# Performance work log

Measured on AMD Instinct MI355X. Metric: run time of the kernel, lower is better.

The kernel has to match this reference:

```python
import jax, jax.numpy as jnp
import numpy as np

B, C, H, W = 4, 64, 256, 256
WIDE = 256      # num_features * width_multiplier
K = 4           # dynamic kernel banks
KS = 3          # kernel size
RED = 16        # channels // reduction = 64 // 4
PAD = KS // 2


def _wn(v, g):
    # torch weight_norm, dim=0: norm over all dims except leading dim
    n = jnp.sqrt(jnp.sum(v * v, axis=tuple(range(1, v.ndim)), keepdims=True))
    return g * v / n


def _conv(x, w, groups=1):
    return jax.lax.conv_general_dilated(
        x, w, window_strides=(1, 1), padding=[(PAD, PAD), (PAD, PAD)],
        feature_group_count=groups, dimension_numbers=('NCHW', 'OIHW', 'NCHW'))


def setup_inputs() -> dict:
    key = jax.random.key(0)
    ks = jax.random.split(key, 16)
    s = lambda k, shape, sc: jax.random.normal(k, shape, jnp.float32) * sc
    return {
        'x': jax.random.normal(ks[0], (B, C, H, W), jnp.float32),
        'scale': jax.random.uniform(ks[1], (B, 1), jnp.float32, 1.0, 4.0),
        # body conv 1 (weight-normed, ReLU)
        'v1': s(ks[2], (WIDE, C, KS, KS), 0.05), 'g1': jnp.ones((WIDE, 1, 1, 1), jnp.float32),
        'b1': jnp.zeros((WIDE,), jnp.float32),
        # body conv 2 (weight-normed, no act)
        'v2': s(ks[3], (C, WIDE, KS, KS), 0.05), 'g2': jnp.ones((C, 1, 1, 1), jnp.float32),
        'b2': jnp.zeros((C,), jnp.float32),
        # scale-aware dynamic conv: K banks of [C_out, C_in, k, k], weight-normed over dim 0 (=K)
        'dyn_v': s(ks[4], (K, C, C, KS, KS), 0.05), 'dyn_g': jnp.ones((K, 1, 1, 1, 1), jnp.float32),
        'dyn_b': jnp.zeros((K, C), jnp.float32),
        # routing: Linear(1 -> K) + softmax
        'att_w': s(ks[5], (1, K), 1.0), 'att_b': jnp.zeros((K,), jnp.float32),
        # SE block: Linear(C -> C/red, no bias), ReLU, Linear(C/red -> C, no bias), Sigmoid
        'se_w1': s(ks[6], (RED, C), 0.1), 'se_w2': s(ks[7], (C, RED), 0.1),
    }


def reference(x, scale, v1, g1, b1, v2, g2, b2, dyn_v, dyn_g, dyn_b,
              att_w, att_b, se_w1, se_w2):
    # --- body: wide weight-normed conv stack ---
    r = jax.nn.relu(_conv(x, _wn(v1, g1)) + b1[None, :, None, None])   # [B,WIDE,H,W]
    r = _conv(r, _wn(v2, g2)) + b2[None, :, None, None]                # [B,C,H,W]
    # --- scale-aware dynamic conv: per-sample softmax mix of K kernels ---
    att = jax.nn.softmax(scale @ att_w + att_b, axis=-1)               # [B,K]
    w_bank = _wn(dyn_v, dyn_g)                                         # [K,C,C,k,k]
    w_b = jnp.einsum('bk,koicd->boicd', att, w_bank)                   # [B,C,C,k,k]
    bias_b = att @ dyn_b                                               # [B,C]
    # batch-grouped conv: one distinct kernel per sample
    y = _conv(r.reshape(1, B * C, H, W), w_b.reshape(B * C, C, KS, KS), groups=B)
    y = y.reshape(B, C, H, W) + bias_b[:, :, None, None]
    # --- SE gating ---
    p = jnp.mean(y, axis=(2, 3))                                       # [B,C]
    gate = jax.nn.sigmoid(jax.nn.relu(p @ se_w1.T) @ se_w2.T)          # [B,C]
    y = y * gate[:, :, None, None]
    # --- residual ---
    return x + y
```

## Files before the change

kernel.cpp:

```cpp
#include <hip/hip_runtime.h>

typedef __attribute__((ext_vector_type(8))) short short8;
typedef __attribute__((ext_vector_type(4))) float f32x4;

#define HH 256
#define WW 256

__device__ inline unsigned int f2bf(float x) {
  unsigned int u = __float_as_uint(x);
  return (u + 0x7fffu + ((u >> 16) & 1u)) >> 16;
}
__device__ inline unsigned int pack2(float a, float b) {
  return f2bf(a) | (f2bf(b) << 16);
}

__global__ __launch_bounds__(256) void xpose_k(const float* __restrict__ x,
                                               unsigned short* __restrict__ xcl) {
  const int t = threadIdx.x;
  const int ci = t & 63;
  const int wv = t >> 6;
  const int x0 = blockIdx.x * 64;
  const int y  = blockIdx.y;
  const int b  = blockIdx.z;
  const float* src = x + ((size_t)(b * 64 + ci) * HH + y) * WW + x0 + wv;
  unsigned short* dst = xcl + ((size_t)(b * HH + y) * WW + x0 + wv) * 64 + ci;
#pragma unroll
  for (int k = 0; k < 16; ++k)
    dst[(size_t)k * 4 * 64] = (unsigned short)f2bf(src[4 * k]);
}

template <int COUT, int CINK>
__global__ __launch_bounds__(256) void wnorm_k(const float* __restrict__ v,
                                               const float* __restrict__ g,
                                               unsigned short* __restrict__ out) {
  constexpr int N = CINK * 9;
  const int co = blockIdx.x, t = threadIdx.x;
  const float* vb = v + (size_t)co * N;
  float s = 0.f;
  for (int i = t; i < N; i += 256) { float a = vb[i]; s += a * a; }
  for (int off = 32; off > 0; off >>= 1) s += __shfl_xor(s, off, 64);
  __shared__ float red[4];
  if ((t & 63) == 0) red[t >> 6] = s;
  __syncthreads();
  const float tot = red[0] + red[1] + red[2] + red[3];
  const float sc = g[co] / sqrtf(tot);
  for (int i = t; i < N; i += 256) {
    int ci = i / 9, tap = i - 9 * (i / 9);
    out[((size_t)tap * COUT + co) * CINK + ci] = (unsigned short)f2bf(vb[i] * sc);
  }
}

__global__ __launch_bounds__(256) void dynnorm_k(const float* __restrict__ dyn_v,
                                                 const float* __restrict__ dyn_g,
                                                 float* __restrict__ dscale) {
  const int k = blockIdx.x, t = threadIdx.x;
  const float* vb = dyn_v + (size_t)k * 36864;
  float s = 0.f;
  for (int i = t; i < 36864; i += 256) { float a = vb[i]; s += a * a; }
  for (int off = 32; off > 0; off >>= 1) s += __shfl_xor(s, off, 64);
  __shared__ float red[4];
  if ((t & 63) == 0) red[t >> 6] = s;
  __syncthreads();
  if (t == 0) dscale[k] = dyn_g[k] / sqrtf(red[0] + red[1] + red[2] + red[3]);
}

__global__ __launch_bounds__(256) void mix_k(const float* __restrict__ scale,
                                             const float* __restrict__ att_w,
                                             const float* __restrict__ att_b,
                                             const float* __restrict__ dyn_v,
                                             const float* __restrict__ dyn_b,
                                             const float* __restrict__ dscale,
                                             unsigned short* __restrict__ wbt,
                                             float* __restrict__ bias_b,
                                             float* __restrict__ zp) {
  const int blk = blockIdx.x;
  const int b = blk >> 6, co = blk & 63;
  const int t = threadIdx.x;
  float att[4], wsc[4];
  const float sc = scale[b];
  float mx = -1e30f;
#pragma unroll
  for (int k = 0; k < 4; ++k) { att[k] = sc * att_w[k] + att_b[k]; mx = fmaxf(mx, att[k]); }
  float den = 0.f;
#pragma unroll
  for (int k = 0; k < 4; ++k) { att[k] = expf(att[k] - mx); den += att[k]; }
#pragma unroll
  for (int k = 0; k < 4; ++k) { att[k] /= den; wsc[k] = att[k] * dscale[k]; }
  for (int i = t; i < 576; i += 256) {
    int ci = i / 9, tap = i - 9 * (i / 9);
    float w = 0.f;
#pragma unroll
    for (int k = 0; k < 4; ++k)
      w += wsc[k] * dyn_v[(((size_t)k * 64 + co) * 64 + ci) * 9 + tap];
    wbt[(((size_t)b * 9 + tap) * 64 + co) * 64 + ci] = (unsigned short)f2bf(w);
  }
  if (t == 0) {
    float bb = 0.f;
#pragma unroll
    for (int k = 0; k < 4; ++k) bb += att[k] * dyn_b[k * 64 + co];
    bias_b[blk] = bb;
  }
  if (blk == 0) zp[t] = 0.f;
}

template <int CIN, int COUT, int OSTR, bool RELU, bool DYN>
__global__ __launch_bounds__(256, 2) void conv3x3_mfma(const unsigned short* __restrict__ in_cl,
                                                       const unsigned short* __restrict__ wt,
                                                       const float* __restrict__ bias,
                                                       unsigned short* __restrict__ out_cl,
                                                       float* __restrict__ y_out,
                                                       float* __restrict__ pblk,
                                                       const float* __restrict__ zp) {
  constexpr int CO_TILES = COUT / 64;
  constexpr int NCH = CIN / 32;
  constexpr int NSLOT = 612 * 4;
  const int tid = threadIdx.x;
  const int lane = tid & 63;
  const int wv = tid >> 6;
  const int l15 = lane & 15;
  const int lg = lane >> 4;

  const int wg = (blockIdx.x & 7) * (gridDim.x >> 3) + (blockIdx.x >> 3);
  int tdec = wg;
  const int cot = tdec % CO_TILES; tdec /= CO_TILES;
  const int bx = tdec & 7; tdec >>= 3;
  const int by = tdec & 15; tdec >>= 4;
  const int bz = tdec;

  const int x0 = bx * 32;
  const int y0 = by * 16;
  const int co0 = cot * 64;

  const unsigned short* inb = in_cl + (size_t)bz * HH * WW * CIN;
  const unsigned short* wtb = wt + (DYN ? (size_t)bz * 9 * 64 * 64 : (size_t)0);
  const float* biasb = bias + (DYN ? bz * 64 : 0);
  const unsigned short* zp16 = (const unsigned short*)zp;

  __shared__ unsigned short tile[NSLOT * 8];
  __shared__ unsigned short atile[2304 * 8];

  const unsigned short* sptr[10];
  bool sact[10];
#pragma unroll
  for (int k = 0; k < 10; ++k) {
    const int u = k * 256 + tid;
    const int pair = u >> 3;
    const int s = ((u & 7) * 16) ^ ((pair & 7) << 4);
    const int parity = s >> 6;
    const int g = (s >> 4) & 3;
    const int px = 2 * pair + parity;
    const int row = px / 34, col = px - 34 * row;
    const int gy = y0 - 1 + row, gx = x0 - 1 + col;
    sact[k] = (u < NSLOT);
    const bool ok = sact[k] && ((unsigned)gy < (unsigned)HH) && ((unsigned)gx < (unsigned)WW);
    sptr[k] = ok ? (inb + ((size_t)(gy * WW + gx)) * CIN + g * 8) : zp16;
  }

  f32x4 acc[4][8];
#pragma unroll
  for (int m = 0; m < 4; ++m)
#pragma unroll
    for (int n = 0; n < 8; ++n) acc[m][n] = (f32x4){0.f, 0.f, 0.f, 0.f};

#pragma unroll 1
  for (int ch = 0; ch < NCH; ++ch) {
    if (ch) __syncthreads();
#pragma unroll
    for (int k = 0; k < 10; ++k) {
      if (sact[k])
        __builtin_amdgcn_global_load_lds((const void*)(sptr[k] + ch * 32),
                                         (void*)(tile + (size_t)(k * 256 + wv * 64) * 8),
                                         16, 0, 0);
    }
#pragma unroll
    for (int k = 0; k < 9; ++k) {
      const int idx = k * 256 + tid;
      const int tap = idx >> 8;
      const int g = (idx >> 6) & 3;
      const int co = idx & 63;
      __builtin_amdgcn_global_load_lds(
          (const void*)(wtb + ((size_t)(tap * COUT + co0 + co) * CIN + ch * 32 + g * 8)),
          (void*)(atile + (size_t)(k * 256 + wv * 64) * 8), 16, 0, 0);
    }
    __syncthreads();

#pragma unroll
    for (int dx = 0; dx < 3; ++dx) {
      short8 Af[3][4];
#pragma unroll
      for (int dy = 0; dy < 3; ++dy)
#pragma unroll
        for (int m = 0; m < 4; ++m)
          Af[dy][m] = *(const short8*)((const char*)atile +
                                       (((dy * 3 + dx) * 4 + lg) * 1024 + (16 * m + l15) * 16));
#pragma unroll
      for (int ch2 = 0; ch2 < 2; ++ch2) {
#pragma unroll
        for (int bi = 0; bi < 6; ++bi) {
          const int px = (4 * wv + bi) * 34 + 16 * ch2 + l15 + dx;
          const int byt = (px >> 1) * 128 + ((lg * 16 + (px & 1) * 64) ^ (((px >> 1) & 7) << 4));
          const short8 Bv = *(const short8*)((const char*)tile + byt);
          const int dy_lo = (bi > 3) ? (bi - 3) : 0;
          const int dy_hi = (bi < 2) ? bi : 2;
          __builtin_amdgcn_s_setprio(1);
#pragma unroll
          for (int dy = 0; dy < 3; ++dy) {
            if (dy < dy_lo || dy > dy_hi) continue;
            const int n = 2 * (bi - dy) + ch2;
#pragma unroll
            for (int m = 0; m < 4; ++m)
              acc[m][n] = __builtin_amdgcn_mfma_f32_16x16x32_bf16(Af[dy][m], Bv, acc[m][n], 0, 0, 0);
          }
          __builtin_amdgcn_s_setprio(0);
        }
      }
    }
  }

  float scol[4][4];
  if (DYN) {
#pragma unroll
    for (int m = 0; m < 4; ++m)
#pragma unroll
      for (int f = 0; f < 4; ++f) scol[m][f] = 0.f;
  }

#pragma unroll
  for (int m = 0; m < 4; ++m) {
    const f32x4 bs = *(const f32x4*)(biasb + co0 + 16 * m + 4 * lg);
#pragma unroll
    for (int n = 0; n < 8; ++n) {
      f32x4 v = acc[m][n] + bs;
      if (RELU) {
        v.x = fmaxf(v.x, 0.f); v.y = fmaxf(v.y, 0.f);
        v.z = fmaxf(v.z, 0.f); v.w = fmaxf(v.w, 0.f);
      }
      const int yy = y0 + 4 * wv + (n >> 1);
      const int xx = x0 + 16 * (n & 1) + l15;
      if (!DYN) {
        uint2 pk;
        pk.x = pack2(v.x, v.y);
        pk.y = pack2(v.z, v.w);
        *(uint2*)(out_cl + (size_t)bz * HH * WW * OSTR +
                  ((size_t)(yy * WW + xx)) * OSTR + co0 + 16 * m + 4 * lg) = pk;
      } else {
        const size_t base = ((size_t)(bz * 64 + 16 * m + 4 * lg) * HH + yy) * WW + xx;
        y_out[base]             = v.x;
        y_out[base + 1 * 65536] = v.y;
        y_out[base + 2 * 65536] = v.z;
        y_out[base + 3 * 65536] = v.w;
        scol[m][0] += v.x; scol[m][1] += v.y; scol[m][2] += v.z; scol[m][3] += v.w;
      }
    }
  }
  if (DYN) {
#pragma unroll
    for (int m = 0; m < 4; ++m)
#pragma unroll
      for (int f = 0; f < 4; ++f) {
        float r = scol[m][f];
        r += __shfl_xor(r, 1, 64);
        r += __shfl_xor(r, 2, 64);
        r += __shfl_xor(r, 4, 64);
        r += __shfl_xor(r, 8, 64);
        scol[m][f] = r;
      }
    __syncthreads();
    float* red = (float*)tile;
    if (l15 == 0) {
#pragma unroll
      for (int m = 0; m < 4; ++m)
#pragma unroll
        for (int f = 0; f < 4; ++f)
          red[wv * 64 + 16 * m + 4 * lg + f] = scol[m][f];
    }
    __syncthreads();
    if (tid < 64) {
      const float s = red[tid] + red[64 + tid] + red[128 + tid] + red[192 + tid];
      pblk[((size_t)bz * 128 + by * 8 + bx) * 64 + tid] = s;
    }
  }
}

__global__ __launch_bounds__(256) void gate_k(const float* __restrict__ pblk,
                                              const float* __restrict__ se_w1,
                                              const float* __restrict__ se_w2,
                                              float* __restrict__ gate) {
  const int b = blockIdx.x;
  const int t = threadIdx.x;
  const int c = t & 63, part = t >> 6;
  __shared__ float ps[4][64];
  __shared__ float p_s[64], h_s[16];
  float s = 0.f;
  for (int blk = part; blk < 128; blk += 4)
    s += pblk[((size_t)b * 128 + blk) * 64 + c];
  ps[part][c] = s;
  __syncthreads();
  if (t < 64) p_s[t] = (ps[0][t] + ps[1][t] + ps[2][t] + ps[3][t]) * (1.f / 65536.f);
  __syncthreads();
  if (t < 16) {
    float h = 0.f;
    for (int cc = 0; cc < 64; ++cc) h += p_s[cc] * se_w1[t * 64 + cc];
    h_s[t] = fmaxf(h, 0.f);
  }
  __syncthreads();
  if (t < 64) {
    float a = 0.f;
    for (int j = 0; j < 16; ++j) a += h_s[j] * se_w2[t * 16 + j];
    gate[b * 64 + t] = 1.f / (1.f + expf(-a));
  }
}

__global__ __launch_bounds__(256) void final_k(const float* __restrict__ x,
                                               const float* __restrict__ gate,
                                               float* __restrict__ out) {
  const size_t i = ((size_t)blockIdx.x * 256 + threadIdx.x) * 4;
  f32x4 yv = *(f32x4*)(out + i);
  const f32x4 xv = *(const f32x4*)(x + i);
  const float g = gate[(int)(i >> 16)];
  yv = xv + yv * g;
  *(f32x4*)(out + i) = yv;
}

static constexpr size_t SZ_XCL = (size_t)4 * 256 * 256 * 64 * 2;
static constexpr size_t SZ_W   = (size_t)9 * 256 * 64 * 2;
static constexpr size_t SZ_PBLK = (size_t)4 * 128 * 64 * 4;

static constexpr size_t B_XCL = 0;
static constexpr size_t B_R   = B_XCL + SZ_XCL;
static constexpr size_t B_W1T = B_R + 4 * SZ_XCL;
static constexpr size_t B_W2T = B_W1T + SZ_W;
static constexpr size_t B_WBT = B_W2T + SZ_W;
static constexpr size_t B_DSC = B_WBT + SZ_W;
static constexpr size_t B_BB  = B_DSC + 256;
static constexpr size_t B_GT  = B_BB + 1024;
static constexpr size_t B_ZP  = B_GT + 1024;
static constexpr size_t B_PBLK = B_ZP + 1024;
static constexpr size_t WS_BIG = B_PBLK + SZ_PBLK;

extern "C" void kernel_launch(void* const* d_in, const int* in_sizes, int n_in,
                              void* d_out, int out_size, void* d_ws, size_t ws_size,
                              hipStream_t stream) {
  (void)in_sizes; (void)n_in; (void)out_size;
  if (ws_size < WS_BIG) return;

  const float* x     = (const float*)d_in[0];
  const float* scale = (const float*)d_in[1];
  const float* v1    = (const float*)d_in[2];
  const float* g1    = (const float*)d_in[3];
  const float* b1    = (const float*)d_in[4];
  const float* v2    = (const float*)d_in[5];
  const float* g2    = (const float*)d_in[6];
  const float* b2    = (const float*)d_in[7];
  const float* dyn_v = (const float*)d_in[8];
  const float* dyn_g = (const float*)d_in[9];
  const float* dyn_b = (const float*)d_in[10];
  const float* att_w = (const float*)d_in[11];
  const float* att_b = (const float*)d_in[12];
  const float* se_w1 = (const float*)d_in[13];
  const float* se_w2 = (const float*)d_in[14];
  float* out = (float*)d_out;

  char* ws = (char*)d_ws;
  unsigned short* xcl  = (unsigned short*)(ws + B_XCL);
  unsigned short* rbuf = (unsigned short*)(ws + B_R);
  unsigned short* r2   = (unsigned short*)(ws + B_XCL);
  unsigned short* w1t  = (unsigned short*)(ws + B_W1T);
  unsigned short* w2t  = (unsigned short*)(ws + B_W2T);
  unsigned short* wbt  = (unsigned short*)(ws + B_WBT);
  float* dscale = (float*)(ws + B_DSC);
  float* bias_b = (float*)(ws + B_BB);
  float* gate   = (float*)(ws + B_GT);
  float* zp     = (float*)(ws + B_ZP);
  float* pblk   = (float*)(ws + B_PBLK);

  xpose_k<<<dim3(4, 256, 4), 256, 0, stream>>>(x, xcl);
  wnorm_k<256, 64><<<256, 256, 0, stream>>>(v1, g1, w1t);
  wnorm_k<64, 256><<<64, 256, 0, stream>>>(v2, g2, w2t);
  dynnorm_k<<<4, 256, 0, stream>>>(dyn_v, dyn_g, dscale);
  mix_k<<<256, 256, 0, stream>>>(scale, att_w, att_b, dyn_v, dyn_b, dscale, wbt, bias_b, zp);

  conv3x3_mfma<64, 256, 256, true, false><<<2048, 256, 0, stream>>>(
      xcl, w1t, b1, rbuf, nullptr, nullptr, zp);
  conv3x3_mfma<256, 64, 64, false, false><<<512, 256, 0, stream>>>(
      rbuf, w2t, b2, r2, nullptr, nullptr, zp);
  conv3x3_mfma<64, 64, 64, false, true><<<512, 256, 0, stream>>>(
      r2, wbt, bias_b, nullptr, out, pblk, zp);

  gate_k<<<4, 256, 0, stream>>>(pblk, se_w1, se_w2, gate);
  final_k<<<16384, 256, 0, stream>>>(x, gate, out);
}
```

Baseline: 356.8 us.

## Double-buffer input tile in LDS and read weights directly from global

The convolution kernel drops the LDS staging buffer for weights and instead loads the A fragments straight from global memory, which relies on the cache. The freed LDS holds a second input tile, so the next channel chunk's async global-to-LDS loads overlap the MFMA work on the current chunk. There is now one barrier per iteration instead of two. The risk is that the global weight loads are uncoalesced and raise register pressure and latency in the inner loop.

Result: slower. 609.7 us (+70.9%).

```diff
diff --git a/kernel.cpp b/kernel.cpp
--- a/kernel.cpp
+++ b/kernel.cpp
@@ -136,11 +136,9 @@
   const float* biasb = bias + (DYN ? bz * 64 : 0);
   const unsigned short* zp16 = (const unsigned short*)zp;
 
-  __shared__ unsigned short tile[NSLOT * 8];
-  __shared__ unsigned short atile[2304 * 8];
+  __shared__ unsigned short tile[2 * NSLOT * 8];
 
   const unsigned short* sptr[10];
-  bool sact[10];
 #pragma unroll
   for (int k = 0; k < 10; ++k) {
     const int u = k * 256 + tid;
@@ -151,8 +149,7 @@
     const int px = 2 * pair + parity;
     const int row = px / 34, col = px - 34 * row;
     const int gy = y0 - 1 + row, gx = x0 - 1 + col;
-    sact[k] = (u < NSLOT);
-    const bool ok = sact[k] && ((unsigned)gy < (unsigned)HH) && ((unsigned)gx < (unsigned)WW);
+    const bool ok = ((unsigned)gy < (unsigned)HH) && ((unsigned)gx < (unsigned)WW);
     sptr[k] = ok ? (inb + ((size_t)(gy * WW + gx)) * CIN + g * 8) : zp16;
   }
 
@@ -161,29 +158,29 @@
   for (int m = 0; m < 4; ++m)
 #pragma unroll
     for (int n = 0; n < 8; ++n) acc[m][n] = (f32x4){0.f, 0.f, 0.f, 0.f};
+
+#pragma unroll
+  for (int k = 0; k < 10; ++k) {
+    if (k < 9 || tid < 144)
+      __builtin_amdgcn_global_load_lds((const void*)(sptr[k]),
+                                       (void*)(tile + (size_t)(k * 256 + wv * 64) * 8),
+                                       16, 0, 0);
+  }
+  __syncthreads();
 
 #pragma unroll 1
   for (int ch = 0; ch < NCH; ++ch) {
-    if (ch) __syncthreads();
-#pragma unroll
-    for (int k = 0; k < 10; ++k) {
-      if (sact[k])
-        __builtin_amdgcn_global_load_lds((const void*)(sptr[k] + ch * 32),
-                                         (void*)(tile + (size_t)(k * 256 + wv * 64) * 8),
-                                         16, 0, 0);
-    }
-#pragma unroll
-    for (int k = 0; k < 9; ++k) {
-      const int idx = k * 256 + tid;
-      const int tap = idx >> 8;
-      const int g = (idx >> 6) & 3;
-      const int co = idx & 63;
-      __builtin_amdgcn_global_load_lds(
-          (const void*)(wtb + ((size_t)(tap * COUT + co0 + co) * CIN + ch * 32 + g * 8)),
-          (void*)(atile + (size_t)(k * 256 + wv * 64) * 8), 16, 0, 0);
-    }
-    __syncthreads();
-
+    const char* cbuf = (const char*)tile + (ch & 1) * (NSLOT * 16);
+    if (ch + 1 < NCH) {
+      unsigned short* dbuf = tile + (size_t)(((ch + 1) & 1)) * NSLOT * 8;
+#pragma unroll
+      for (int k = 0; k < 10; ++k) {
+        if (k < 9 || tid < 144)
+          __builtin_amdgcn_global_load_lds((const void*)(sptr[k] + (ch + 1) * 32),
+                                           (void*)(dbuf + (size_t)(k * 256 + wv * 64) * 8),
+                                           16, 0, 0);
+      }
+    }
 #pragma unroll
     for (int dx = 0; dx < 3; ++dx) {
       short8 Af[3][4];
@@ -191,15 +188,15 @@
       for (int dy = 0; dy < 3; ++dy)
 #pragma unroll
         for (int m = 0; m < 4; ++m)
-          Af[dy][m] = *(const short8*)((const char*)atile +
-                                       (((dy * 3 + dx) * 4 + lg) * 1024 + (16 * m + l15) * 16));
+          Af[dy][m] = *(const short8*)(wtb + (((size_t)((dy * 3 + dx) * COUT + co0 + 16 * m + l15)) * CIN +
+                                              ch * 32 + lg * 8));
 #pragma unroll
       for (int ch2 = 0; ch2 < 2; ++ch2) {
 #pragma unroll
         for (int bi = 0; bi < 6; ++bi) {
           const int px = (4 * wv + bi) * 34 + 16 * ch2 + l15 + dx;
           const int byt = (px >> 1) * 128 + ((lg * 16 + (px & 1) * 64) ^ (((px >> 1) & 7) << 4));
-          const short8 Bv = *(const short8*)((const char*)tile + byt);
+          const short8 Bv = *(const short8*)(cbuf + byt);
           const int dy_lo = (bi > 3) ? (bi - 3) : 0;
           const int dy_hi = (bi < 2) ? bi : 2;
           __builtin_amdgcn_s_setprio(1);
@@ -215,6 +212,7 @@
         }
       }
     }
+    __syncthreads();
   }
 
   float scol[4][4];
```
